# Kernel optimization log

Hardware: AMD Instinct MI355X
Metric: run time of the kernel (lower is better)

The kernel has to match this reference:

```python
import jax, jax.numpy as jnp
import numpy as np

B, I, H = 512, 2048, 2048


def setup_inputs() -> dict:
    key = jax.random.key(0)
    ks = jax.random.split(key, 14)
    s = 0.02  # weight init scale
    inp = {
        "inputs": jax.random.normal(ks[0], (B, I), jnp.float32),
        "states": jax.random.normal(ks[1], (2, B, H), jnp.float32),
        "Wi": jax.random.normal(ks[2], (I, H), jnp.float32) * s,
        "Ui": jax.random.normal(ks[3], (H, H), jnp.float32) * s,
        "bi": jnp.zeros((H,), jnp.float32),
        "Wf": jax.random.normal(ks[4], (I, H), jnp.float32) * s,
        "Uf": jax.random.normal(ks[5], (H, H), jnp.float32) * s,
        "bf": jnp.zeros((H,), jnp.float32),
        "Wg": jax.random.normal(ks[6], (I, H), jnp.float32) * s,
        "Ug": jax.random.normal(ks[7], (H, H), jnp.float32) * s,
        "bg": jnp.zeros((H,), jnp.float32),
        "Wc": jax.random.normal(ks[8], (I, H), jnp.float32) * s,
        "Uc": jax.random.normal(ks[9], (H, H), jnp.float32) * s,
        "bc": jnp.zeros((H,), jnp.float32),
    }
    return inp


def reference(inputs, states, Wi, Ui, bi, Wf, Uf, bf, Wg, Ug, bg, Wc, Uc, bc):
    # Faithful to the original cell, including its quirks:
    # recurrent matmuls use states[0] (prevstate); c mixes states[1] (prevoutput).
    prevstate, prevoutput = states[0], states[1]  # [B,H] each
    i = jax.nn.sigmoid(inputs @ Wi + prevstate @ Ui + bi)
    f = jax.nn.sigmoid(inputs @ Wf + prevstate @ Uf + bf)
    g = jax.nn.sigmoid(inputs @ Wg + prevstate @ Ug + bg)
    c_ = jnp.tanh(inputs @ Wc + prevstate @ Uc + bc)
    c = f * prevoutput + i * c_
    state = g * jnp.tanh(c)
    return c, jnp.stack([state, c])
```

## Files before the change

kernel.cpp:

```cpp
#include <hip/hip_runtime.h>
#include <hip/hip_bf16.h>

#define BH (512*2048)
#define LDT 40
#define PPLANE (512ull*8192ull)

typedef __attribute__((ext_vector_type(8))) short short8;
typedef __attribute__((ext_vector_type(4))) float floatx4;
typedef __attribute__((ext_vector_type(4))) unsigned short ushort4v;
typedef __attribute__((ext_vector_type(8))) unsigned short ushort8v;

__device__ inline unsigned short f2bf(float x){
    unsigned u = __builtin_bit_cast(unsigned, x);
    return (unsigned short)((u + 0x7fffu + ((u >> 16) & 1u)) >> 16);
}
__device__ inline float bf2f(unsigned short s){
    unsigned u = ((unsigned)s) << 16;
    return __builtin_bit_cast(float, u);
}
__device__ inline float fsig(float x){
    return __builtin_amdgcn_rcpf(1.f + __expf(-x));
}
__device__ inline float ftanh(float x){
    return 2.f * fsig(2.f * x) - 1.f;
}

__global__ __launch_bounds__(512, 1) void gemm_half(
    const float* __restrict__ inputs, const float* __restrict__ states,
    const float* __restrict__ Wi, const float* __restrict__ Ui,
    const float* __restrict__ Wf, const float* __restrict__ Uf,
    const float* __restrict__ Wg, const float* __restrict__ Ug,
    const float* __restrict__ Wc, const float* __restrict__ Uc,
    unsigned short* __restrict__ P)
{
    __shared__ unsigned short As[128 * LDT];
    __shared__ unsigned short Bs[128 * LDT];

    const int t    = threadIdx.x;
    const int m0   = blockIdx.y * 128;
    const int z    = blockIdx.z;
    const int nblk = blockIdx.x;
    const int gate = nblk >> 4;
    const int c0   = (nblk & 15) * 128;

    const float* Bsel;
    if (z == 0) {
        switch (gate) { case 0: Bsel = Wi; break; case 1: Bsel = Wf; break;
                        case 2: Bsel = Wg; break; default: Bsel = Wc; }
    } else {
        switch (gate) { case 0: Bsel = Ui; break; case 1: Bsel = Uf; break;
                        case 2: Bsel = Ug; break; default: Bsel = Uc; }
    }
    const float* Abase = (z == 0) ? inputs : states;

    const int lane  = t & 63;
    const int wave  = t >> 6;
    const int wm    = (wave & 3) * 32;
    const int wn    = (wave >> 2) * 64;
    const int row16 = lane & 15;
    const int oct   = lane >> 4;

    const int a_c4 = t & 7;
    const int a_r0 = t >> 3;
    const int b_n   = t & 127;
    const int b_oct = t >> 7;

    floatx4 acc[2][4];
    #pragma unroll
    for (int i = 0; i < 2; i++)
        #pragma unroll
        for (int j = 0; j < 4; j++)
            acc[i][j] = (floatx4){0.f, 0.f, 0.f, 0.f};

    for (int kk = 0; kk < 64; kk++) {
        const int k0 = kk * 32;
        const float* aptr = Abase + (size_t)m0 * 2048 + k0;
        const float* bptr = Bsel + (size_t)k0 * 2048 + c0;

        floatx4 av0 = *(const floatx4*)(aptr + (size_t)a_r0 * 2048 + a_c4 * 4);
        floatx4 av1 = *(const floatx4*)(aptr + (size_t)(a_r0 + 64) * 2048 + a_c4 * 4);
        float bv[8];
        #pragma unroll
        for (int j = 0; j < 8; j++)
            bv[j] = bptr[(size_t)(b_oct * 8 + j) * 2048 + b_n];

        __syncthreads();

        ushort4v w0, w1;
        #pragma unroll
        for (int j = 0; j < 4; j++) { w0[j] = f2bf(av0[j]); w1[j] = f2bf(av1[j]); }
        *(ushort4v*)&As[a_r0 * LDT + a_c4 * 4]        = w0;
        *(ushort4v*)&As[(a_r0 + 64) * LDT + a_c4 * 4] = w1;
        ushort8v wb;
        #pragma unroll
        for (int j = 0; j < 8; j++) wb[j] = f2bf(bv[j]);
        *(ushort8v*)&Bs[b_n * LDT + b_oct * 8] = wb;

        __syncthreads();

        short8 af[2], bfr[4];
        #pragma unroll
        for (int mi = 0; mi < 2; mi++)
            af[mi] = *(const short8*)&As[(wm + mi * 16 + row16) * LDT + oct * 8];
        #pragma unroll
        for (int ni = 0; ni < 4; ni++)
            bfr[ni] = *(const short8*)&Bs[(wn + ni * 16 + row16) * LDT + oct * 8];
        #pragma unroll
        for (int mi = 0; mi < 2; mi++)
            #pragma unroll
            for (int ni = 0; ni < 4; ni++)
                acc[mi][ni] = __builtin_amdgcn_mfma_f32_16x16x32_bf16(
                    af[mi], bfr[ni], acc[mi][ni], 0, 0, 0);
    }

    unsigned short* dst = P + (size_t)z * PPLANE;
    const int gbase = gate * 2048 + c0;
    #pragma unroll
    for (int mi = 0; mi < 2; mi++)
        #pragma unroll
        for (int ni = 0; ni < 4; ni++)
            #pragma unroll
            for (int j = 0; j < 4; j++) {
                int row = m0 + wm + mi * 16 + oct * 4 + j;
                int col = gbase + wn + ni * 16 + row16;
                dst[(size_t)row * 8192 + col] = f2bf(acc[mi][ni][j]);
            }
}

__global__ __launch_bounds__(256) void combine_kernel(
    float* __restrict__ out, const unsigned short* __restrict__ P,
    const float* __restrict__ states,
    const float* __restrict__ bi, const float* __restrict__ bfv,
    const float* __restrict__ bg, const float* __restrict__ bc)
{
    const int idx = (blockIdx.x * 256 + threadIdx.x) * 8;
    const int row = idx >> 11;
    const int h   = idx & 2047;
    const size_t base = (size_t)row * 8192 + h;
    const unsigned short* P1 = P + PPLANE;
    const float* po = states + BH;

    ushort8v ai0 = *(const ushort8v*)&P [base];
    ushort8v ai1 = *(const ushort8v*)&P1[base];
    ushort8v af0 = *(const ushort8v*)&P [base + 2048];
    ushort8v af1 = *(const ushort8v*)&P1[base + 2048];
    ushort8v ag0 = *(const ushort8v*)&P [base + 4096];
    ushort8v ag1 = *(const ushort8v*)&P1[base + 4096];
    ushort8v ac0 = *(const ushort8v*)&P [base + 6144];
    ushort8v ac1 = *(const ushort8v*)&P1[base + 6144];

    floatx4 pov[2], vbi[2], vbf[2], vbg[2], vbc[2];
    #pragma unroll
    for (int q = 0; q < 2; q++) {
        pov[q] = *(const floatx4*)&po [idx + q * 4];
        vbi[q] = *(const floatx4*)&bi [h + q * 4];
        vbf[q] = *(const floatx4*)&bfv[h + q * 4];
        vbg[q] = *(const floatx4*)&bg [h + q * 4];
        vbc[q] = *(const floatx4*)&bc [h + q * 4];
    }

    floatx4 vc[2], vs[2];
    #pragma unroll
    for (int q = 0; q < 2; q++)
        #pragma unroll
        for (int j = 0; j < 4; j++) {
            int e = q * 4 + j;
            float xi = bf2f(ai0[e]) + bf2f(ai1[e]) + vbi[q][j];
            float xf = bf2f(af0[e]) + bf2f(af1[e]) + vbf[q][j];
            float xg = bf2f(ag0[e]) + bf2f(ag1[e]) + vbg[q][j];
            float xc = bf2f(ac0[e]) + bf2f(ac1[e]) + vbc[q][j];
            float c  = fsig(xf) * pov[q][j] + fsig(xi) * ftanh(xc);
            vc[q][j] = c;
            vs[q][j] = fsig(xg) * ftanh(c);
        }
    #pragma unroll
    for (int q = 0; q < 2; q++) {
        *(floatx4*)&out[idx + q * 4]          = vc[q];
        *(floatx4*)&out[BH + idx + q * 4]     = vs[q];
        *(floatx4*)&out[2 * BH + idx + q * 4] = vc[q];
    }
}

extern "C" void kernel_launch(void* const* d_in, const int* in_sizes, int n_in,
                              void* d_out, int out_size, void* d_ws, size_t ws_size,
                              hipStream_t stream) {
    const float* inputs = (const float*)d_in[0];
    const float* states = (const float*)d_in[1];
    const float* Wi = (const float*)d_in[2];
    const float* Ui = (const float*)d_in[3];
    const float* bi = (const float*)d_in[4];
    const float* Wf = (const float*)d_in[5];
    const float* Uf = (const float*)d_in[6];
    const float* bf = (const float*)d_in[7];
    const float* Wg = (const float*)d_in[8];
    const float* Ug = (const float*)d_in[9];
    const float* bg = (const float*)d_in[10];
    const float* Wc = (const float*)d_in[11];
    const float* Uc = (const float*)d_in[12];
    const float* bc = (const float*)d_in[13];
    float* out = (float*)d_out;
    unsigned short* P = (unsigned short*)d_ws;

    dim3 grid(64, 4, 2);
    gemm_half<<<grid, 512, 0, stream>>>(inputs, states, Wi, Ui, Wf, Uf,
                                        Wg, Ug, Wc, Uc, P);
    combine_kernel<<<BH / (8 * 256), 256, 0, stream>>>(out, P, states, bi, bf, bg, bc);
}
```

Baseline: 241.6 us.

## Double-buffer LDS GEMM with swizzle, 4x4 wave tiles, and split-K over planes

Rewrites the GEMM kernel to stage the next K-slice in registers while MFMAs run on the current LDS buffer, which removes one barrier per iteration. It also swizzles the LDS layout to avoid bank conflicts and gives each wave a 64x64 tile with 256 threads and two blocks per CU. When the workspace is large enough, K is split into four slices to raise parallelism, and the combine kernel sums a variable number of partial planes. Conversion now uses cheaper round-half-up packing via perm instead of round-to-nearest-even. The trade-offs are more partial-plane traffic and slightly different rounding.

```diff
diff --git a/kernel.cpp b/kernel.cpp
--- a/kernel.cpp
+++ b/kernel.cpp
@@ -1,40 +1,40 @@
 #include <hip/hip_runtime.h>
-#include <hip/hip_bf16.h>
 
 #define BH (512*2048)
-#define LDT 40
 #define PPLANE (512ull*8192ull)
+#define PLANE_BYTES (PPLANE*2ull)
 
 typedef __attribute__((ext_vector_type(8))) short short8;
 typedef __attribute__((ext_vector_type(4))) float floatx4;
-typedef __attribute__((ext_vector_type(4))) unsigned short ushort4v;
+typedef __attribute__((ext_vector_type(4))) unsigned int uint4v;
 typedef __attribute__((ext_vector_type(8))) unsigned short ushort8v;
 
-__device__ inline unsigned short f2bf(float x){
-    unsigned u = __builtin_bit_cast(unsigned, x);
-    return (unsigned short)((u + 0x7fffu + ((u >> 16) & 1u)) >> 16);
+__device__ inline unsigned pk2(float a, float b){
+    unsigned ua = __builtin_bit_cast(unsigned, a) + 0x8000u;
+    unsigned ub = __builtin_bit_cast(unsigned, b) + 0x8000u;
+    return __builtin_amdgcn_perm(ub, ua, 0x07060302u);
+}
+__device__ inline unsigned short f2bf1(float x){
+    return (unsigned short)((__builtin_bit_cast(unsigned, x) + 0x8000u) >> 16);
 }
 __device__ inline float bf2f(unsigned short s){
-    unsigned u = ((unsigned)s) << 16;
-    return __builtin_bit_cast(float, u);
-}
-__device__ inline float fsig(float x){
-    return __builtin_amdgcn_rcpf(1.f + __expf(-x));
-}
-__device__ inline float ftanh(float x){
-    return 2.f * fsig(2.f * x) - 1.f;
-}
-
-__global__ __launch_bounds__(512, 1) void gemm_half(
+    return __builtin_bit_cast(float, ((unsigned)s) << 16);
+}
+__device__ inline int swz(int r, int g){ return r*4 + (g ^ ((r>>1)&3)); }
+
+__device__ inline float fsig(float x){ return __builtin_amdgcn_rcpf(1.f + __expf(-x)); }
+__device__ inline float ftanh(float x){ return 2.f*fsig(2.f*x) - 1.f; }
+
+__global__ __launch_bounds__(256, 2) void gemm_tile(
     const float* __restrict__ inputs, const float* __restrict__ states,
     const float* __restrict__ Wi, const float* __restrict__ Ui,
     const float* __restrict__ Wf, const float* __restrict__ Uf,
     const float* __restrict__ Wg, const float* __restrict__ Ug,
     const float* __restrict__ Wc, const float* __restrict__ Uc,
-    unsigned short* __restrict__ P)
+    unsigned short* __restrict__ P, int KB)
 {
-    __shared__ unsigned short As[128 * LDT];
-    __shared__ unsigned short Bs[128 * LDT];
+    __shared__ uint4v As[2][512];
+    __shared__ uint4v Bs[2][512];
 
     const int t    = threadIdx.x;
     const int m0   = blockIdx.y * 128;
@@ -42,88 +42,117 @@
     const int nblk = blockIdx.x;
     const int gate = nblk >> 4;
     const int c0   = (nblk & 15) * 128;
-
-    const float* Bsel;
-    if (z == 0) {
-        switch (gate) { case 0: Bsel = Wi; break; case 1: Bsel = Wf; break;
-                        case 2: Bsel = Wg; break; default: Bsel = Wc; }
+    const int gk   = z * KB;
+
+    const float* Abase; const float* Bsel; int ko;
+    if (gk < 2048) {
+        Abase = inputs; ko = gk;
+        switch (gate){ case 0: Bsel=Wi; break; case 1: Bsel=Wf; break;
+                       case 2: Bsel=Wg; break; default: Bsel=Wc; }
     } else {
-        switch (gate) { case 0: Bsel = Ui; break; case 1: Bsel = Uf; break;
-                        case 2: Bsel = Ug; break; default: Bsel = Uc; }
-    }
-    const float* Abase = (z == 0) ? inputs : states;
+        Abase = states; ko = gk - 2048;
+        switch (gate){ case 0: Bsel=Ui; break; case 1: Bsel=Uf; break;
+                       case 2: Bsel=Ug; break; default: Bsel=Uc; }
+    }
+    const int NIT = KB >> 5;
 
     const int lane  = t & 63;
     const int wave  = t >> 6;
-    const int wm    = (wave & 3) * 32;
-    const int wn    = (wave >> 2) * 64;
+    const int wm    = (wave & 1) * 64;
+    const int wn    = (wave >> 1) * 64;
     const int row16 = lane & 15;
-    const int oct   = lane >> 4;
-
-    const int a_c4 = t & 7;
-    const int a_r0 = t >> 3;
-    const int b_n   = t & 127;
-    const int b_oct = t >> 7;
-
-    floatx4 acc[2][4];
-    #pragma unroll
-    for (int i = 0; i < 2; i++)
+    const int g4    = lane >> 4;
+
+    const int ar  = t >> 2;
+    const int ag  = t & 3;
+    const int bn  = t & 127;
+    const int bg2 = (t >> 7) * 2;
+
+    const float* Ap = Abase + (size_t)(m0 + ar) * 2048 + ko + ag * 8;
+    const float* Bp = Bsel  + (size_t)ko * 2048 + c0 + bn;
+
+    floatx4 acc[4][4];
+    #pragma unroll
+    for (int i = 0; i < 4; i++)
         #pragma unroll
         for (int j = 0; j < 4; j++)
-            acc[i][j] = (floatx4){0.f, 0.f, 0.f, 0.f};
-
-    for (int kk = 0; kk < 64; kk++) {
-        const int k0 = kk * 32;
-        const float* aptr = Abase + (size_t)m0 * 2048 + k0;
-        const float* bptr = Bsel + (size_t)k0 * 2048 + c0;
-
-        floatx4 av0 = *(const floatx4*)(aptr + (size_t)a_r0 * 2048 + a_c4 * 4);
-        floatx4 av1 = *(const floatx4*)(aptr + (size_t)(a_r0 + 64) * 2048 + a_c4 * 4);
-        float bv[8];
-        #pragma unroll
-        for (int j = 0; j < 8; j++)
-            bv[j] = bptr[(size_t)(b_oct * 8 + j) * 2048 + b_n];
-
+            acc[i][j] = (floatx4){0.f,0.f,0.f,0.f};
+
+    floatx4 a0,a1,a2,a3;
+    float b0[8], b1[8];
+
+    a0 = *(const floatx4*)Ap;            a1 = *(const floatx4*)(Ap + 4);
+    a2 = *(const floatx4*)(Ap + 64*2048); a3 = *(const floatx4*)(Ap + 64*2048 + 4);
+    #pragma unroll
+    for (int j = 0; j < 8; j++) b0[j] = Bp[(size_t)(bg2*8 + j) * 2048];
+    #pragma unroll
+    for (int j = 0; j < 8; j++) b1[j] = Bp[(size_t)(bg2*8 + 8 + j) * 2048];
+    {
+        uint4v w;
+        w.x=pk2(a0[0],a0[1]); w.y=pk2(a0[2],a0[3]); w.z=pk2(a1[0],a1[1]); w.w=pk2(a1[2],a1[3]);
+        As[0][swz(ar, ag)] = w;
+        w.x=pk2(a2[0],a2[1]); w.y=pk2(a2[2],a2[3]); w.z=pk2(a3[0],a3[1]); w.w=pk2(a3[2],a3[3]);
+        As[0][swz(ar+64, ag)] = w;
+        w.x=pk2(b0[0],b0[1]); w.y=pk2(b0[2],b0[3]); w.z=pk2(b0[4],b0[5]); w.w=pk2(b0[6],b0[7]);
+        Bs[0][swz(bn, bg2)] = w;
+        w.x=pk2(b1[0],b1[1]); w.y=pk2(b1[2],b1[3]); w.z=pk2(b1[4],b1[5]); w.w=pk2(b1[6],b1[7]);
+        Bs[0][swz(bn, bg2+1)] = w;
+    }
+
+    for (int kk = 0; kk < NIT; kk++) {
         __syncthreads();
-
-        ushort4v w0, w1;
-        #pragma unroll
-        for (int j = 0; j < 4; j++) { w0[j] = f2bf(av0[j]); w1[j] = f2bf(av1[j]); }
-        *(ushort4v*)&As[a_r0 * LDT + a_c4 * 4]        = w0;
-        *(ushort4v*)&As[(a_r0 + 64) * LDT + a_c4 * 4] = w1;
-        ushort8v wb;
-        #pragma unroll
-        for (int j = 0; j < 8; j++) wb[j] = f2bf(bv[j]);
-        *(ushort8v*)&Bs[b_n * LDT + b_oct * 8] = wb;
-
-        __syncthreads();
-
-        short8 af[2], bfr[4];
-        #pragma unroll
-        for (int mi = 0; mi < 2; mi++)
-            af[mi] = *(const short8*)&As[(wm + mi * 16 + row16) * LDT + oct * 8];
+        const int cur = kk & 1;
+
+        if (kk + 1 < NIT) {
+            const float* ap = Ap + (kk+1) * 32;
+            a0 = *(const floatx4*)ap;             a1 = *(const floatx4*)(ap + 4);
+            a2 = *(const floatx4*)(ap + 64*2048); a3 = *(const floatx4*)(ap + 64*2048 + 4);
+            const float* bp = Bp + (size_t)(kk+1) * 32 * 2048;
+            #pragma unroll
+            for (int j = 0; j < 8; j++) b0[j] = bp[(size_t)(bg2*8 + j) * 2048];
+            #pragma unroll
+            for (int j = 0; j < 8; j++) b1[j] = bp[(size_t)(bg2*8 + 8 + j) * 2048];
+        }
+
+        short8 afr[4], bfr[4];
+        #pragma unroll
+        for (int mi = 0; mi < 4; mi++)
+            afr[mi] = *(const short8*)&As[cur][swz(wm + mi*16 + row16, g4)];
         #pragma unroll
         for (int ni = 0; ni < 4; ni++)
-            bfr[ni] = *(const short8*)&Bs[(wn + ni * 16 + row16) * LDT + oct * 8];
-        #pragma unroll
-        for (int mi = 0; mi < 2; mi++)
+            bfr[ni] = *(const short8*)&Bs[cur][swz(wn + ni*16 + row16, g4)];
+        #pragma unroll
+        for (int mi = 0; mi < 4; mi++)
             #pragma unroll
             for (int ni = 0; ni < 4; ni++)
                 acc[mi][ni] = __builtin_amdgcn_mfma_f32_16x16x32_bf16(
-                    af[mi], bfr[ni], acc[mi][ni], 0, 0, 0);
+                    afr[mi], bfr[ni], acc[mi][ni], 0, 0, 0);
+
+        if (kk + 1 < NIT) {
+            const int nxt = cur ^ 1;
+            uint4v w;
+            w.x=pk2(a0[0],a0[1]); w.y=pk2(a0[2],a0[3]); w.z=pk2(a1[0],a1[1]); w.w=pk2(a1[2],a1[3]);
+            As[nxt][swz(ar, ag)] = w;
+            w.x=pk2(a2[0],a2[1]); w.y=pk2(a2[2],a2[3]); w.z=pk2(a3[0],a3[1]); w.w=pk2(a3[2],a3[3]);
+            As[nxt][swz(ar+64, ag)] = w;
+            w.x=pk2(b0[0],b0[1]); w.y=pk2(b0[2],b0[3]); w.z=pk2(b0[4],b0[5]); w.w=pk2(b0[6],b0[7]);
+            Bs[nxt][swz(bn, bg2)] = w;
+            w.x=pk2(b1[0],b1[1]); w.y=pk2(b1[2],b1[3]); w.z=pk2(b1[4],b1[5]); w.w=pk2(b1[6],b1[7]);
+            Bs[nxt][swz(bn, bg2+1)] = w;
+        }
     }
 
     unsigned short* dst = P + (size_t)z * PPLANE;
     const int gbase = gate * 2048 + c0;
     #pragma unroll
-    for (int mi = 0; mi < 2; mi++)
+    for (int mi = 0; mi < 4; mi++)
         #pragma unroll
         for (int ni = 0; ni < 4; ni++)
             #pragma unroll
             for (int j = 0; j < 4; j++) {
-                int row = m0 + wm + mi * 16 + oct * 4 + j;
-                int col = gbase + wn + ni * 16 + row16;
-                dst[(size_t)row * 8192 + col] = f2bf(acc[mi][ni][j]);
+                int row = m0 + wm + mi*16 + g4*4 + j;
+                int col = gbase + wn + ni*16 + row16;
+                dst[(size_t)row * 8192 + col] = f2bf1(acc[mi][ni][j]);
             }
 }
 
@@ -131,53 +160,51 @@
     float* __restrict__ out, const unsigned short* __restrict__ P,
     const float* __restrict__ states,
     const float* __restrict__ bi, const float* __restrict__ bfv,
-    const float* __restrict__ bg, const float* __restrict__ bc)
+    const float* __restrict__ bg, const float* __restrict__ bc, int nz)
 {
     const int idx = (blockIdx.x * 256 + threadIdx.x) * 8;
     const int row = idx >> 11;
     const int h   = idx & 2047;
     const size_t base = (size_t)row * 8192 + h;
-    const unsigned short* P1 = P + PPLANE;
+
+    float xi[8], xf[8], xg[8], xc[8];
+    #pragma unroll
+    for (int e = 0; e < 8; e++) {
+        xi[e] = bi[h+e]; xf[e] = bfv[h+e]; xg[e] = bg[h+e]; xc[e] = bc[h+e];
+    }
+    for (int z = 0; z < nz; z++) {
+        const unsigned short* Pz = P + (size_t)z * PPLANE;
+        ushort8v vi = *(const ushort8v*)&Pz[base];
+        ushort8v vf = *(const ushort8v*)&Pz[base + 2048];
+        ushort8v vg = *(const ushort8v*)&Pz[base + 4096];
+        ushort8v vc = *(const ushort8v*)&Pz[base + 6144];
+        #pragma unroll
+        for (int e = 0; e < 8; e++) {
+            xi[e] += bf2f(vi[e]); xf[e] += bf2f(vf[e]);
+            xg[e] += bf2f(vg[e]); xc[e] += bf2f(vc[e]);
+        }
+    }
+
     const float* po = states + BH;
-
-    ushort8v ai0 = *(const ushort8v*)&P [base];
-    ushort8v ai1 = *(const ushort8v*)&P1[base];
-    ushort8v af0 = *(const ushort8v*)&P [base + 2048];
-    ushort8v af1 = *(const ushort8v*)&P1[base + 2048];
-    ushort8v ag0 = *(const ushort8v*)&P [base + 4096];
-    ushort8v ag1 = *(const ushort8v*)&P1[base + 4096];
-    ushort8v ac0 = *(const ushort8v*)&P [base + 6144];
-    ushort8v ac1 = *(const ushort8v*)&P1[base + 6144];
-
-    floatx4 pov[2], vbi[2], vbf[2], vbg[2], vbc[2];
+    floatx4 pov[2];
+    pov[0] = *(const floatx4*)&po[idx];
+    pov[1] = *(const floatx4*)&po[idx + 4];
+
+    floatx4 vcv[2], vsv[2];
+    #pragma unroll
+    for (int q = 0; q < 2; q++)
+        #pragma unroll
+        for (int j = 0; j < 4; j++) {
+            int e = q*4 + j;
+            float c = fsig(xf[e]) * pov[q][j] + fsig(xi[e]) * ftanh(xc[e]);
+            vcv[q][j] = c;
+            vsv[q][j] = fsig(xg[e]) * ftanh(c);
+        }
     #pragma unroll
     for (int q = 0; q < 2; q++) {
-        pov[q] = *(const floatx4*)&po [idx + q * 4];
-        vbi[q] = *(const floatx4*)&bi [h + q * 4];
-        vbf[q] = *(const floatx4*)&bfv[h + q * 4];
-        vbg[q] = *(const floatx4*)&bg [h + q * 4];
-        vbc[q] = *(const floatx4*)&bc [h + q * 4];
-    }
-
-    floatx4 vc[2], vs[2];
-    #pragma unroll
-    for (int q = 0; q < 2; q++)
-        #pragma unroll
-        for (int j = 0; j < 4; j++) {
-            int e = q * 4 + j;
-            float xi = bf2f(ai0[e]) + bf2f(ai1[e]) + vbi[q][j];
-            float xf = bf2f(af0[e]) + bf2f(af1[e]) + vbf[q][j];
-            float xg = bf2f(ag0[e]) + bf2f(ag1[e]) + vbg[q][j];
-            float xc = bf2f(ac0[e]) + bf2f(ac1[e]) + vbc[q][j];
-            float c  = fsig(xf) * pov[q][j] + fsig(xi) * ftanh(xc);
-            vc[q][j] = c;
-            vs[q][j] = fsig(xg) * ftanh(c);
-        }
-    #pragma unroll
-    for (int q = 0; q < 2; q++) {
-        *(floatx4*)&out[idx + q * 4]          = vc[q];
-        *(floatx4*)&out[BH + idx + q * 4]     = vs[q];
-        *(floatx4*)&out[2 * BH + idx + q * 4] = vc[q];
+        *(floatx4*)&out[idx + q*4]          = vcv[q];
+        *(floatx4*)&out[BH + idx + q*4]     = vsv[q];
+        *(floatx4*)&out[2*BH + idx + q*4]   = vcv[q];
     }
 }
 
@@ -201,8 +228,12 @@
     float* out = (float*)d_out;
     unsigned short* P = (unsigned short*)d_ws;
 
-    dim3 grid(64, 4, 2);
-    gemm_half<<<grid, 512, 0, stream>>>(inputs, states, Wi, Ui, Wf, Uf,
-                                        Wg, Ug, Wc, Uc, P);
-    combine_kernel<<<BH / (8 * 256), 256, 0, stream>>>(out, P, states, bi, bf, bg, bc);
-}
+    const int nz = (ws_size >= 4 * PLANE_BYTES) ? 4 : 2;
+    const int KB = 4096 / nz;
+
+    dim3 grid(64, 4, nz);
+    gemm_tile<<<grid, 256, 0, stream>>>(inputs, states, Wi, Ui, Wf, Uf,
+                                        Wg, Ug, Wc, Uc, P, KB);
+    combine_kernel<<<BH / (8 * 256), 256, 0, stream>>>(out, P, states,
+                                                       bi, bf, bg, bc, nz);
+}
```

Result: no change. 238.1 us (-1.4%).
